# Kernel tuning notes

Measured on AMD Instinct MI355X. Metric: run time of the kernel, lower is better.

## Reference

```python
import jax, jax.numpy as jnp
import numpy as np
import math

B, I, H, NH, HD, OUT = 65536, 256, 64, 8, 8, 64


def _lin(z, W, b):
    # torch nn.Linear convention: W is [out, in]
    return z @ W.T + b


def setup_inputs() -> dict:
    key = jax.random.key(0)
    ks = jax.random.split(key, 30)
    n = lambda i, shape, s=1.0: (jax.random.normal(ks[i], shape, dtype=jnp.float32) * s)
    inp = {
        "x": n(0, (B, I)),
        # _compute_persistence returns random diagrams independent of x; materialized as input
        "persistence": n(1, (I, B, 3, 2)),
        "topo_kernel": n(2, (H, I, 3), 0.05),
        "q_w": n(3, (H, H), 0.05), "q_b": n(4, (H,), 0.05),
        "k_w": n(5, (H, H), 0.05), "k_b": n(6, (H,), 0.05),
        "v_w": n(7, (H, H), 0.05), "v_b": n(8, (H,), 0.05),
        "o_w": n(9, (H, H), 0.05), "o_b": n(10, (H,), 0.05),
        "phase": n(11, (NH,)),
        "update_w": n(12, (H, 2 * H), 0.05), "update_b": n(13, (H,), 0.05),
        "reset_w": n(14, (H, 2 * H), 0.05), "reset_b": n(15, (H,), 0.05),
        "state_w": n(16, (H, 2 * H), 0.05), "state_b": n(17, (H,), 0.05),
        "fisher_m": n(18, (H, H)),
        "metric_m": n(19, (H, H), 0.1),
        "connection": n(20, (H, H, H), 0.01),
        "proj_w": n(21, (H, H), 0.05), "proj_b": n(22, (H,), 0.05),
        "obj_emb": n(23, (H, 64), 0.05),
        "morphisms": n(24, (H, 64, 64), 0.05),
        "functor_w": n(25, (H,)),
        "out_w": n(26, (OUT, 64), 0.05), "out_b": n(27, (OUT,), 0.05),
    }
    return inp


def reference(x, persistence, topo_kernel, q_w, q_b, k_w, k_b, v_w, v_b, o_w, o_b,
              phase, update_w, update_b, reset_w, reset_b, state_w, state_b,
              fisher_m, metric_m, connection, proj_w, proj_b,
              obj_emb, morphisms, functor_w, out_w, out_b):
    # ---- TopologicalConv: out[b,o] = sum_j sum_{d,t} pers[j][b,d,t] * kernel[o,j,d]
    topo = jnp.einsum('jbdt,ojd->bo', persistence, topo_kernel)  # [B, H]

    # ---- QuantumAttentionLayer (seq_len = 1, heads act as the attended axis)
    q = _lin(topo, q_w, q_b).reshape(-1, NH, HD)
    k = _lin(topo, k_w, k_b).reshape(-1, NH, HD)
    v = _lin(topo, v_w, v_b).reshape(-1, NH, HD)
    ph = jnp.exp(1j * phase)[None, :, None]            # per-head phase rotation
    qc = q * ph
    kc = k * jnp.conj(ph)
    scores = jnp.einsum('bhd,bgd->bhg', qc, kc) / math.sqrt(HD)  # [B, NH, NH] complex
    attn = jax.nn.softmax(scores.real, axis=-1) + 1j * jax.nn.softmax(scores.imag, axis=-1)
    av = jnp.einsum('bhg,bgd->bhd', attn, v.astype(attn.dtype))
    quantum = _lin(av.real.reshape(-1, H), o_w, o_b)   # [B, H]

    # ---- InformationRNN single step with h0 = 0
    h0 = jnp.zeros_like(quantum)
    combined = jnp.concatenate([quantum, h0], axis=1)
    update = jax.nn.sigmoid(_lin(combined, update_w, update_b))
    reset = jax.nn.sigmoid(_lin(combined, reset_w, reset_b))
    state_in = jnp.concatenate([quantum, reset * h0], axis=1)
    cand = jnp.tanh(_lin(state_in, state_w, state_b))
    fisher = fisher_m @ fisher_m.T
    nat_grad = jnp.linalg.solve(fisher, (cand - h0).T).T  # fisher @ g = (cand - h)
    new_h = (1.0 - update) * h0 + update * (h0 + nat_grad)

    # ---- ManifoldLayer (geodesic distances are computed-then-discarded in source; skipped)
    metric = metric_m @ metric_m.T
    xm = new_h @ metric
    transported = xm + jnp.einsum('bi,bj,ijk->bk', xm, xm, connection)
    manifold = _lin(transported, proj_w, proj_b)

    # ---- CategoryTheoryNetwork: sum_m softmax(w)_m * (obj @ M_m) == obj @ (sum_m w_m M_m)
    obj = manifold @ obj_emb                     # [B, 64]
    fw = jax.nn.softmax(functor_w)
    m_eff = jnp.einsum('m,mij->ij', fw, morphisms)
    cat = obj @ m_eff                            # [B, 64]

    return _lin(cat, out_w, out_b)               # [B, OUT]
```

## Files before the change

### kernel.cpp

```cpp
#include <hip/hip_runtime.h>
#include <math.h>

typedef float f32x4 __attribute__((ext_vector_type(4)));
typedef __bf16 bf16x8 __attribute__((ext_vector_type(8)));
typedef unsigned short u16x8 __attribute__((ext_vector_type(8)));

__device__ __forceinline__ unsigned short f2bf(float f) {
  unsigned u = __float_as_uint(f);
  return (unsigned short)((u + 0x7fffu + ((u >> 16) & 1u)) >> 16);
}
__device__ __forceinline__ float bf2f(unsigned short s) {
  return __uint_as_float(((unsigned)s) << 16);
}
__device__ __forceinline__ void unpk(unsigned v, float& a, float& b) {
  a = __uint_as_float(v << 16);
  b = __uint_as_float(v & 0xffff0000u);
}
__device__ __forceinline__ bf16x8 ld8bf(const unsigned short* p) {
  uint4 u = *(const uint4*)p;
  return __builtin_bit_cast(bf16x8, u);
}
__device__ __forceinline__ bf16x8 pack8(const float* f) {
  u16x8 t;
#pragma unroll
  for (int i = 0; i < 8; ++i) t[i] = f2bf(f[i]);
  return __builtin_bit_cast(bf16x8, t);
}
__device__ __forceinline__ bf16x8 ld8f32(const float* p) {
  float4 a = *(const float4*)p;
  float4 b = *(const float4*)(p + 4);
  float f[8] = {a.x, a.y, a.z, a.w, b.x, b.y, b.z, b.w};
  return pack8(f);
}
__device__ __forceinline__ f32x4 mfma16(bf16x8 a, bf16x8 b, f32x4 c) {
  return __builtin_amdgcn_mfma_f32_16x16x32_bf16(a, b, c, 0, 0, 0);
}

#define TOPO_OFF   0u
#define CENDT_OFF  8388608u
#define FINV_OFF   8921088u
#define MET_OFF    8929280u
#define WU_OFF     8937472u
#define WC_OFF     8945664u
#define WENDF_OFF  8953856u
#define BU_OFF     8970240u
#define BC_OFF     8970496u
#define BEND_OFF   8970752u
#define COSD_OFF   8971008u

__global__ __launch_bounds__(256, 4) void k_setup_topo(
    const float* __restrict__ pers, const float* __restrict__ tk,
    const float* __restrict__ fisher_m, const float* __restrict__ morphisms,
    const float* __restrict__ functor_w, const float* __restrict__ obj_emb,
    const float* __restrict__ out_w, const float* __restrict__ proj_w,
    const float* __restrict__ proj_b, const float* __restrict__ out_b,
    const float* __restrict__ update_w, const float* __restrict__ update_b,
    const float* __restrict__ state_w, const float* __restrict__ state_b,
    const float* __restrict__ o_w, const float* __restrict__ o_b,
    const float* __restrict__ metric_m, const float* __restrict__ phase,
    char* __restrict__ ws)
{
  __shared__ char smem[33280];
  const int bid = blockIdx.x, tid = threadIdx.x;

  if (bid < 1024) {
    unsigned short* p2 = (unsigned short*)smem;
    const int w = tid >> 6, lane = tid & 63;
    const int m = lane & 15, quad = lane >> 4;
    const size_t b0 = (size_t)bid * 64;
    f32x4 acc[4] = {};
    for (int chunk = 0; chunk < 8; ++chunk) {
      __syncthreads();
#pragma unroll
      for (int rr = 0; rr < 4; ++rr) {
        const int jl = rr * 8 + (tid >> 5);
        const int j = chunk * 32 + jl;
        const int b = (tid & 31) * 2;
        const float4* src = (const float4*)(pers + ((size_t)j * 65536 + b0 + b) * 6);
        float4 f0 = src[0], f1 = src[1], f2c = src[2];
        const int k0 = jl * 3;
        unsigned short* r0p = p2 + b * 104 + k0;
        unsigned short* r1p = p2 + (b + 1) * 104 + k0;
        r0p[0] = f2bf(f0.x + f0.y);
        r0p[1] = f2bf(f0.z + f0.w);
        r0p[2] = f2bf(f1.x + f1.y);
        r1p[0] = f2bf(f1.z + f1.w);
        r1p[1] = f2bf(f2c.x + f2c.y);
        r1p[2] = f2bf(f2c.z + f2c.w);
      }
      __syncthreads();
#pragma unroll
      for (int ks = 0; ks < 3; ++ks) {
        bf16x8 a = ld8bf(p2 + (w * 16 + m) * 104 + ks * 32 + quad * 8);
        const int kg = chunk * 96 + ks * 32 + quad * 8;
#pragma unroll
        for (int nt = 0; nt < 4; ++nt) {
          bf16x8 bb = ld8f32(tk + (nt * 16 + m) * 768 + kg);
          acc[nt] = mfma16(a, bb, acc[nt]);
        }
      }
    }
    unsigned short* topo_bf = (unsigned short*)(ws + TOPO_OFF);
#pragma unroll
    for (int nt = 0; nt < 4; ++nt)
#pragma unroll
      for (int r = 0; r < 4; ++r)
        topo_bf[(b0 + w * 16 + quad * 4 + r) * 64 + nt * 16 + m] = f2bf(acc[nt][r]);

  } else if (bid == 1024) {
    float* aug = (float*)smem;
    for (int e = tid; e < 4096; e += 256) {
      const int r = e >> 6, c = e & 63;
      float s = 0.f;
      for (int l = 0; l < 64; ++l) s += fisher_m[r * 64 + l] * fisher_m[c * 64 + l];
      aug[r * 130 + c] = s;
      aug[r * 130 + 64 + c] = (r == c) ? 1.f : 0.f;
    }
    __syncthreads();
    const int rr = tid >> 2, cs = tid & 3;
    for (int p = 0; p < 64; ++p) {
      const float piv = 1.f / aug[p * 130 + p];
      const float f = (rr != p) ? aug[rr * 130 + p] : 0.f;
      __syncthreads();
      if (tid < 130) aug[p * 130 + tid] *= piv;
      __syncthreads();
      if (rr != p)
        for (int c = cs; c < 130; c += 4)
          aug[rr * 130 + c] -= f * aug[p * 130 + c];
      __syncthreads();
    }
    unsigned short* finv = (unsigned short*)(ws + FINV_OFF);
    for (int e = tid; e < 4096; e += 256)
      finv[e] = f2bf(aug[(e >> 6) * 130 + 64 + (e & 63)]);

  } else if (bid == 1025) {
    float* L0 = (float*)smem;
    float* L1s = (float*)(smem + 16384);
    float* fw = (float*)(smem + 32768);
    if (tid < 64) {
      float mx = functor_w[0];
      for (int i2 = 1; i2 < 64; ++i2) mx = fmaxf(mx, functor_w[i2]);
      float se = 0.f;
      for (int i2 = 0; i2 < 64; ++i2) se += expf(functor_w[i2] - mx);
      fw[tid] = expf(functor_w[tid] - mx) / se;
    }
    __syncthreads();
    for (int e = tid; e < 4096; e += 256) {
      const int p = e >> 6, q = e & 63;
      float s = 0.f;
      for (int m2 = 0; m2 < 64; ++m2) s += fw[m2] * morphisms[m2 * 4096 + p * 64 + q];
      L0[e] = s;
    }
    __syncthreads();
    for (int e = tid; e < 4096; e += 256) {
      const int mm2 = e >> 6, q = e & 63;
      float s = 0.f;
      for (int p = 0; p < 64; ++p) s += obj_emb[mm2 * 64 + p] * L0[p * 64 + q];
      L1s[e] = s;
    }
    __syncthreads();
    for (int e = tid; e < 4096; e += 256) {
      const int mm2 = e >> 6, n = e & 63;
      float s = 0.f;
      for (int q = 0; q < 64; ++q) s += L1s[mm2 * 64 + q] * out_w[n * 64 + q];
      L0[e] = s;
    }
    __syncthreads();
    float* wendf = (float*)(ws + WENDF_OFF);
    for (int e = tid; e < 4096; e += 256) {
      const int kp = e >> 6, n = e & 63;
      float s = 0.f;
      for (int m2 = 0; m2 < 64; ++m2) s += proj_w[m2 * 64 + kp] * L0[m2 * 64 + n];
      wendf[e] = s;
    }
    if (tid < 64) {
      float s = out_b[tid];
      for (int m2 = 0; m2 < 64; ++m2) s += proj_b[m2] * L0[m2 * 64 + tid];
      ((float*)(ws + BEND_OFF))[tid] = s;
    }

  } else {
    unsigned short* wu = (unsigned short*)(ws + WU_OFF);
    unsigned short* wc = (unsigned short*)(ws + WC_OFF);
    unsigned short* met = (unsigned short*)(ws + MET_OFF);
    for (int e = tid; e < 4096; e += 256) {
      const int n = e >> 6, k2 = e & 63;
      float su = 0.f, sc = 0.f, sm = 0.f;
      for (int m2 = 0; m2 < 64; ++m2) {
        const float ow = o_w[m2 * 64 + k2];
        su += update_w[n * 128 + m2] * ow;
        sc += state_w[n * 128 + m2] * ow;
        sm += metric_m[n * 64 + m2] * metric_m[k2 * 64 + m2];
      }
      wu[e] = f2bf(su); wc[e] = f2bf(sc); met[e] = f2bf(sm);
    }
    if (tid < 64) {
      float s1 = update_b[tid], s2 = state_b[tid];
      for (int m2 = 0; m2 < 64; ++m2) {
        const float ob = o_b[m2];
        s1 += update_w[tid * 128 + m2] * ob;
        s2 += state_w[tid * 128 + m2] * ob;
      }
      ((float*)(ws + BU_OFF))[tid] = s1;
      ((float*)(ws + BC_OFF))[tid] = s2;
    } else if (tid < 128) {
      const int e = tid - 64;
      ((float*)(ws + COSD_OFF))[e] =
          cosf(phase[e >> 3] - phase[e & 7]) * 0.35355339059327376f;
    }
  }
}

__global__ __launch_bounds__(256) void k_cend(const float* __restrict__ conn,
                                              char* __restrict__ ws)
{
  __shared__ float wl[4096];
  const int bid = blockIdx.x, tid = threadIdx.x;
  unsigned short* cendt = (unsigned short*)(ws + CENDT_OFF);
  const float* wendf = (const float*)(ws + WENDF_OFF);
  if (bid < 64) {
    for (int e = tid; e < 4096; e += 256) wl[e] = wendf[e];
    __syncthreads();
    const int i = bid;
    const int j = tid >> 2, nb = tid & 3;
    float cr[64];
    const float* cp = conn + ((size_t)i * 64 + j) * 64;
#pragma unroll
    for (int kp = 0; kp < 64; ++kp) cr[kp] = cp[kp];
    for (int n = nb * 16; n < nb * 16 + 16; ++n) {
      float s = 0.f;
#pragma unroll
      for (int kp = 0; kp < 64; ++kp) s += cr[kp] * wl[kp * 64 + n];
      cendt[(size_t)n * 4160 + i * 64 + j] = f2bf(s);
    }
  } else {
    for (int e = tid; e < 4096; e += 256) {
      const int i2 = e >> 6, n = e & 63;
      cendt[(size_t)n * 4160 + 4096 + i2] = f2bf(wendf[i2 * 64 + n]);
    }
  }
}

__global__ __launch_bounds__(256, 2) void k_main(
    const float* __restrict__ q_w, const float* __restrict__ q_b,
    const float* __restrict__ k_w, const float* __restrict__ k_b,
    const float* __restrict__ v_w, const float* __restrict__ v_b,
    const char* __restrict__ ws, float* __restrict__ out)
{
  __shared__ char smem[73728];
  unsigned short* S0 = (unsigned short*)smem;
  unsigned short* S1 = (unsigned short*)(smem + 18432);
  unsigned short* S2 = (unsigned short*)(smem + 36864);
  unsigned short* S3 = (unsigned short*)(smem + 55296);
  const int tid = threadIdx.x;
  const int w = tid >> 6, lane = tid & 63;
  const int m = lane & 15, quad = lane >> 4;
  const size_t r0 = (size_t)blockIdx.x * 128;
  const unsigned short* topo_bf = (const unsigned short*)(ws + TOPO_OFF);
  const unsigned short* CENDT = (const unsigned short*)(ws + CENDT_OFF);
  const unsigned short* FINV = (const unsigned short*)(ws + FINV_OFF);
  const unsigned short* MET = (const unsigned short*)(ws + MET_OFF);
  const unsigned short* WU = (const unsigned short*)(ws + WU_OFF);
  const unsigned short* WC = (const unsigned short*)(ws + WC_OFF);
  const float* BU = (const float*)(ws + BU_OFF);
  const float* BC = (const float*)(ws + BC_OFF);
  const float* BEND = (const float*)(ws + BEND_OFF);
  const float* COSD = (const float*)(ws + COSD_OFF);

  {
    const float* Wp[3] = {q_w, k_w, v_w};
    const float* Bp[3] = {q_b, k_b, v_b};
    unsigned short* Dp[3] = {S0, S1, S2};
#pragma unroll
    for (int g3 = 0; g3 < 3; ++g3) {
      bf16x8 bfr[2][4];
#pragma unroll
      for (int ks = 0; ks < 2; ++ks)
#pragma unroll
        for (int nt = 0; nt < 4; ++nt)
          bfr[ks][nt] = ld8f32(Wp[g3] + (nt * 16 + m) * 64 + ks * 32 + quad * 8);
      float bias[4];
#pragma unroll
      for (int nt = 0; nt < 4; ++nt) bias[nt] = Bp[g3][nt * 16 + m];
#pragma unroll
      for (int mi = 0; mi < 2; ++mi) {
        const int mt = w * 2 + mi;
        f32x4 acc[4] = {};
#pragma unroll
        for (int ks = 0; ks < 2; ++ks) {
          bf16x8 a = ld8bf(topo_bf + (r0 + mt * 16 + m) * 64 + ks * 32 + quad * 8);
#pragma unroll
          for (int nt = 0; nt < 4; ++nt) acc[nt] = mfma16(a, bfr[ks][nt], acc[nt]);
        }
#pragma unroll
        for (int nt = 0; nt < 4; ++nt)
#pragma unroll
          for (int r = 0; r < 4; ++r)
            Dp[g3][(mt * 16 + quad * 4 + r) * 72 + nt * 16 + m] =
                f2bf(acc[nt][r] + bias[nt]);
      }
    }
  }
  __syncthreads();

  {
    const int bl = tid >> 1, hh = (tid & 1) * 4;
    float kvv[64];
    const uint4* krow = (const uint4*)(S1 + bl * 72);
#pragma unroll
    for (int x = 0; x < 8; ++x) {
      uint4 u = krow[x];
      unpk(u.x, kvv[x * 8 + 0], kvv[x * 8 + 1]);
      unpk(u.y, kvv[x * 8 + 2], kvv[x * 8 + 3]);
      unpk(u.z, kvv[x * 8 + 4], kvv[x * 8 + 5]);
      unpk(u.w, kvv[x * 8 + 6], kvv[x * 8 + 7]);
    }
    const uint4* qrow = (const uint4*)(S0 + bl * 72);
    const uint4* vrow = (const uint4*)(S2 + bl * 72);
#pragma unroll
    for (int hi = 0; hi < 4; ++hi) {
      const int h = hh + hi;
      float qv[8];
      {
        uint4 u = qrow[h];
        unpk(u.x, qv[0], qv[1]); unpk(u.y, qv[2], qv[3]);
        unpk(u.z, qv[4], qv[5]); unpk(u.w, qv[6], qv[7]);
      }
      float s[8];
#pragma unroll
      for (int g = 0; g < 8; ++g) {
        float a = 0.f;
#pragma unroll
        for (int d = 0; d < 8; ++d) a += qv[d] * kvv[g * 8 + d];
        s[g] = a * COSD[h * 8 + g];
      }
      float mx = s[0];
#pragma unroll
      for (int g = 1; g < 8; ++g) mx = fmaxf(mx, s[g]);
      float se = 0.f;
#pragma unroll
      for (int g = 0; g < 8; ++g) { s[g] = expf(s[g] - mx); se += s[g]; }
      const float inv = 1.f / se;
      float av[8] = {};
#pragma unroll
      for (int g = 0; g < 8; ++g) {
        const float ag = s[g] * inv;
        float vg[8];
        uint4 u = vrow[g];
        unpk(u.x, vg[0], vg[1]); unpk(u.y, vg[2], vg[3]);
        unpk(u.z, vg[4], vg[5]); unpk(u.w, vg[6], vg[7]);
#pragma unroll
        for (int d = 0; d < 8; ++d) av[d] += ag * vg[d];
      }
      unsigned int* dstp = (unsigned int*)(S3 + bl * 72 + h * 8);
#pragma unroll
      for (int d2 = 0; d2 < 4; ++d2)
        dstp[d2] = (unsigned)f2bf(av[2 * d2]) | ((unsigned)f2bf(av[2 * d2 + 1]) << 16);
    }
  }
  __syncthreads();

  {
#pragma unroll
    for (int g2 = 0; g2 < 2; ++g2) {
      const unsigned short* wp = g2 ? WC : WU;
      const float* bp = g2 ? BC : BU;
      unsigned short* dst = g2 ? S1 : S0;
      bf16x8 bfr[2][4];
#pragma unroll
      for (int ks = 0; ks < 2; ++ks)
#pragma unroll
        for (int nt = 0; nt < 4; ++nt)
          bfr[ks][nt] = ld8bf(wp + (nt * 16 + m) * 64 + ks * 32 + quad * 8);
      float bias[4];
#pragma unroll
      for (int nt = 0; nt < 4; ++nt) bias[nt] = bp[nt * 16 + m];
#pragma unroll
      for (int mi = 0; mi < 2; ++mi) {
        const int mt = w * 2 + mi;
        f32x4 acc[4] = {};
#pragma unroll
        for (int ks = 0; ks < 2; ++ks) {
          bf16x8 a = ld8bf(S3 + (mt * 16 + m) * 72 + ks * 32 + quad * 8);
#pragma unroll
          for (int nt = 0; nt < 4; ++nt) acc[nt] = mfma16(a, bfr[ks][nt], acc[nt]);
        }
#pragma unroll
        for (int nt = 0; nt < 4; ++nt)
#pragma unroll
          for (int r = 0; r < 4; ++r) {
            const float x = acc[nt][r] + bias[nt];
            const float y = g2 ? tanhf(x) : 1.f / (1.f + expf(-x));
            dst[(mt * 16 + quad * 4 + r) * 72 + nt * 16 + m] = f2bf(y);
          }
      }
    }
  }
  __syncthreads();

  {
    bf16x8 bfr[2][4];
#pragma unroll
    for (int ks = 0; ks < 2; ++ks)
#pragma unroll
      for (int nt = 0; nt < 4; ++nt)
        bfr[ks][nt] = ld8bf(FINV + (nt * 16 + m) * 64 + ks * 32 + quad * 8);
#pragma unroll
    for (int mi = 0; mi < 2; ++mi) {
      const int mt = w * 2 + mi;
      f32x4 acc[4] = {};
#pragma unroll
      for (int ks = 0; ks < 2; ++ks) {
        bf16x8 a = ld8bf(S1 + (mt * 16 + m) * 72 + ks * 32 + quad * 8);
#pragma unroll
        for (int nt = 0; nt < 4; ++nt) acc[nt] = mfma16(a, bfr[ks][nt], acc[nt]);
      }
#pragma unroll
      for (int nt = 0; nt < 4; ++nt)
#pragma unroll
        for (int r = 0; r < 4; ++r) {
          const int row = mt * 16 + quad * 4 + r, col = nt * 16 + m;
          const float u = bf2f(S0[row * 72 + col]);
          S2[row * 72 + col] = f2bf(u * acc[nt][r]);
        }
    }
  }
  __syncthreads();

  {
    float* XM = (float*)smem;
    bf16x8 bfr[2][4];
#pragma unroll
    for (int ks = 0; ks < 2; ++ks)
#pragma unroll
      for (int nt = 0; nt < 4; ++nt)
        bfr[ks][nt] = ld8bf(MET + (nt * 16 + m) * 64 + ks * 32 + quad * 8);
#pragma unroll
    for (int mi = 0; mi < 2; ++mi) {
      const int mt = w * 2 + mi;
      f32x4 acc[4] = {};
#pragma unroll
      for (int ks = 0; ks < 2; ++ks) {
        bf16x8 a = ld8bf(S2 + (mt * 16 + m) * 72 + ks * 32 + quad * 8);
#pragma unroll
        for (int nt = 0; nt < 4; ++nt) acc[nt] = mfma16(a, bfr[ks][nt], acc[nt]);
      }
#pragma unroll
      for (int nt = 0; nt < 4; ++nt)
#pragma unroll
        for (int r = 0; r < 4; ++r)
          XM[(mt * 16 + quad * 4 + r) * 68 + nt * 16 + m] = acc[nt][r];
    }
  }
  __syncthreads();

  {
    float* XM = (float*)smem;
    unsigned short* stg = (unsigned short*)(smem + 36864);
    float seg[2][2][8];
#pragma unroll
    for (int mi = 0; mi < 2; ++mi) {
      const int brow = w * 32 + mi * 16 + m;
#pragma unroll
      for (int s = 0; s < 2; ++s)
#pragma unroll
        for (int jj = 0; jj < 8; ++jj)
          seg[mi][s][jj] = XM[brow * 68 + s * 32 + quad * 8 + jj];
    }
    f32x4 acc2[2][4] = {};

    auto stage = [&](int cc, int half) {
#pragma unroll
      for (int ks = 0; ks < 4; ++ks) {
        const unsigned short* gp =
            CENDT + (size_t)(w * 16 + m) * 4160 + cc * 128 + ks * 32 + quad * 8;
        const char* lp = smem + 36864 + half * 16384 + (ks * 4 + w) * 1024;
        __builtin_amdgcn_global_load_lds(
            (const __attribute__((address_space(1))) unsigned int*)gp,
            (__attribute__((address_space(3))) unsigned int*)lp, 16, 0, 0);
      }
    };

    stage(0, 0);
    for (int cc = 0; cc < 32; ++cc) {
      __syncthreads();
      if (cc + 1 < 32) stage(cc + 1, (cc + 1) & 1);
      const unsigned short* buf = stg + (cc & 1) * 8192;
#pragma unroll
      for (int ks = 0; ks < 4; ++ks) {
        const int i = cc * 2 + (ks >> 1);
        const int s = ks & 1;
        bf16x8 afr[2];
#pragma unroll
        for (int mi = 0; mi < 2; ++mi) {
          const float xi = XM[(w * 32 + mi * 16 + m) * 68 + i];
          float pr[8];
#pragma unroll
          for (int jj = 0; jj < 8; ++jj) pr[jj] = xi * seg[mi][s][jj];
          afr[mi] = pack8(pr);
        }
#pragma unroll
        for (int nt = 0; nt < 4; ++nt) {
          bf16x8 bfr = ld8bf(buf + (ks * 4 + nt) * 512 + lane * 8);
          acc2[0][nt] = mfma16(afr[0], bfr, acc2[0][nt]);
          acc2[1][nt] = mfma16(afr[1], bfr, acc2[1][nt]);
        }
      }
    }
#pragma unroll
    for (int ks = 0; ks < 2; ++ks) {
      bf16x8 afr[2];
#pragma unroll
      for (int mi = 0; mi < 2; ++mi) afr[mi] = pack8(seg[mi][ks]);
#pragma unroll
      for (int nt = 0; nt < 4; ++nt) {
        bf16x8 bfr =
            ld8bf(CENDT + (size_t)(nt * 16 + m) * 4160 + 4096 + ks * 32 + quad * 8);
        acc2[0][nt] = mfma16(afr[0], bfr, acc2[0][nt]);
        acc2[1][nt] = mfma16(afr[1], bfr, acc2[1][nt]);
      }
    }
    float bendv[4];
#pragma unroll
    for (int nt = 0; nt < 4; ++nt) bendv[nt] = BEND[nt * 16 + m];
#pragma unroll
    for (int mi = 0; mi < 2; ++mi)
#pragma unroll
      for (int nt = 0; nt < 4; ++nt)
#pragma unroll
        for (int r = 0; r < 4; ++r)
          out[(r0 + (w * 2 + mi) * 16 + quad * 4 + r) * 64 + nt * 16 + m] =
              acc2[mi][nt][r] + bendv[nt];
  }
}

extern "C" void kernel_launch(void* const* d_in, const int* in_sizes, int n_in,
                              void* d_out, int out_size, void* d_ws, size_t ws_size,
                              hipStream_t stream) {
  (void)in_sizes; (void)n_in; (void)out_size; (void)ws_size;
  const float* pers     = (const float*)d_in[1];
  const float* tk       = (const float*)d_in[2];
  const float* q_w      = (const float*)d_in[3];
  const float* q_b      = (const float*)d_in[4];
  const float* k_w      = (const float*)d_in[5];
  const float* k_b      = (const float*)d_in[6];
  const float* v_w      = (const float*)d_in[7];
  const float* v_b      = (const float*)d_in[8];
  const float* o_w      = (const float*)d_in[9];
  const float* o_b      = (const float*)d_in[10];
  const float* phase    = (const float*)d_in[11];
  const float* update_w = (const float*)d_in[12];
  const float* update_b = (const float*)d_in[13];
  const float* state_w  = (const float*)d_in[16];
  const float* state_b  = (const float*)d_in[17];
  const float* fisher_m = (const float*)d_in[18];
  const float* metric_m = (const float*)d_in[19];
  const float* conn     = (const float*)d_in[20];
  const float* proj_w   = (const float*)d_in[21];
  const float* proj_b   = (const float*)d_in[22];
  const float* obj_emb  = (const float*)d_in[23];
  const float* morph    = (const float*)d_in[24];
  const float* funct_w  = (const float*)d_in[25];
  const float* out_w    = (const float*)d_in[26];
  const float* out_b    = (const float*)d_in[27];
  char* ws = (char*)d_ws;

  hipLaunchKernelGGL(k_setup_topo, dim3(1027), dim3(256), 0, stream,
                     pers, tk, fisher_m, morph, funct_w, obj_emb, out_w, proj_w,
                     proj_b, out_b, update_w, update_b, state_w, state_b, o_w,
                     o_b, metric_m, phase, ws);
  hipLaunchKernelGGL(k_cend, dim3(65), dim3(256), 0, stream, conn, ws);
  hipLaunchKernelGGL(k_main, dim3(512), dim3(256), 0, stream,
                     q_w, q_b, k_w, k_b, v_w, v_b, (const char*)ws,
                     (float*)d_out);
}
```

Baseline: 922.8 us.

## Load persistence directly into MFMA registers and prepack topo kernel to bf16

The topological conv stage no longer stages persistence through shared memory with block barriers. Each lane loads its own row's persistence values straight into registers, prefetching the next k-step while the current MFMA runs, and pads each group of 3 to 4 so a K-slice of 8 covers two j indices. A new small kernel pre-converts topo_kernel into a padded bf16 layout in workspace, replacing per-iteration fp32 loads and conversions. In exchange the global reads are small float2 loads per lane (64 rows times stride 24 bytes) instead of wide float4 loads, there is an extra kernel launch, and the MFMA work grows by a third because of the zero padding.

```diff
diff --git a/kernel.cpp b/kernel.cpp
--- a/kernel.cpp
+++ b/kernel.cpp
@@ -47,6 +47,15 @@
 #define BC_OFF     8970496u
 #define BEND_OFF   8970752u
 #define COSD_OFF   8971008u
+#define TKP_OFF    8971264u
+
+__global__ __launch_bounds__(256) void k_pretk(const float* __restrict__ tk,
+                                               char* __restrict__ ws) {
+  const int e = blockIdx.x * 256 + threadIdx.x;
+  const int o = e >> 10, kk = e & 1023, j = kk >> 2, d = kk & 3;
+  const float v = (d < 3) ? tk[((size_t)o * 256 + j) * 3 + d] : 0.f;
+  ((unsigned short*)(ws + TKP_OFF))[e] = f2bf(v);
+}
 
 __global__ __launch_bounds__(256, 4) void k_setup_topo(
     const float* __restrict__ pers, const float* __restrict__ tk,
@@ -64,40 +73,45 @@
   const int bid = blockIdx.x, tid = threadIdx.x;
 
   if (bid < 1024) {
-    unsigned short* p2 = (unsigned short*)smem;
     const int w = tid >> 6, lane = tid & 63;
     const int m = lane & 15, quad = lane >> 4;
-    const size_t b0 = (size_t)bid * 64;
+    const size_t rowbase = (size_t)bid * 64 + w * 16;
+    const size_t b = rowbase + m;
+    const unsigned short* tkp = (const unsigned short*)(ws + TKP_OFF);
+    const float* pbase = pers + b * 6;
+
     f32x4 acc[4] = {};
-    for (int chunk = 0; chunk < 8; ++chunk) {
-      __syncthreads();
-#pragma unroll
-      for (int rr = 0; rr < 4; ++rr) {
-        const int jl = rr * 8 + (tid >> 5);
-        const int j = chunk * 32 + jl;
-        const int b = (tid & 31) * 2;
-        const float4* src = (const float4*)(pers + ((size_t)j * 65536 + b0 + b) * 6);
-        float4 f0 = src[0], f1 = src[1], f2c = src[2];
-        const int k0 = jl * 3;
-        unsigned short* r0p = p2 + b * 104 + k0;
-        unsigned short* r1p = p2 + (b + 1) * 104 + k0;
-        r0p[0] = f2bf(f0.x + f0.y);
-        r0p[1] = f2bf(f0.z + f0.w);
-        r0p[2] = f2bf(f1.x + f1.y);
-        r1p[0] = f2bf(f1.z + f1.w);
-        r1p[1] = f2bf(f2c.x + f2c.y);
-        r1p[2] = f2bf(f2c.z + f2c.w);
-      }
-      __syncthreads();
-#pragma unroll
-      for (int ks = 0; ks < 3; ++ks) {
-        bf16x8 a = ld8bf(p2 + (w * 16 + m) * 104 + ks * 32 + quad * 8);
-        const int kg = chunk * 96 + ks * 32 + quad * 8;
-#pragma unroll
-        for (int nt = 0; nt < 4; ++nt) {
-          bf16x8 bb = ld8f32(tk + (nt * 16 + m) * 768 + kg);
-          acc[nt] = mfma16(a, bb, acc[nt]);
-        }
+    float2 c0, c1, c2, c3, c4, c5;
+    {
+      const float* p0 = pbase + (size_t)(quad * 2) * 393216;
+      c0 = *(const float2*)(p0);
+      c1 = *(const float2*)(p0 + 2);
+      c2 = *(const float2*)(p0 + 4);
+      const float* p1 = p0 + 393216;
+      c3 = *(const float2*)(p1);
+      c4 = *(const float2*)(p1 + 2);
+      c5 = *(const float2*)(p1 + 4);
+    }
+    for (int ks = 0; ks < 32; ++ks) {
+      float f[8] = {c0.x + c0.y, c1.x + c1.y, c2.x + c2.y, 0.f,
+                    c3.x + c3.y, c4.x + c4.y, c5.x + c5.y, 0.f};
+      bf16x8 a = pack8(f);
+      if (ks + 1 < 32) {
+        const int jn = (ks + 1) * 8 + quad * 2;
+        const float* p0 = pbase + (size_t)jn * 393216;
+        c0 = *(const float2*)(p0);
+        c1 = *(const float2*)(p0 + 2);
+        c2 = *(const float2*)(p0 + 4);
+        const float* p1 = p0 + 393216;
+        c3 = *(const float2*)(p1);
+        c4 = *(const float2*)(p1 + 2);
+        c5 = *(const float2*)(p1 + 4);
+      }
+      const unsigned short* bk = tkp + ks * 32 + quad * 8;
+#pragma unroll
+      for (int nt = 0; nt < 4; ++nt) {
+        bf16x8 bb = ld8bf(bk + (size_t)(nt * 16 + m) * 1024);
+        acc[nt] = mfma16(a, bb, acc[nt]);
       }
     }
     unsigned short* topo_bf = (unsigned short*)(ws + TOPO_OFF);
@@ -105,7 +119,7 @@
     for (int nt = 0; nt < 4; ++nt)
 #pragma unroll
       for (int r = 0; r < 4; ++r)
-        topo_bf[(b0 + w * 16 + quad * 4 + r) * 64 + nt * 16 + m] = f2bf(acc[nt][r]);
+        topo_bf[(rowbase + quad * 4 + r) * 64 + nt * 16 + m] = f2bf(acc[nt][r]);
 
   } else if (bid == 1024) {
     float* aug = (float*)smem;
@@ -565,6 +579,7 @@
   const float* out_b    = (const float*)d_in[27];
   char* ws = (char*)d_ws;
 
+  hipLaunchKernelGGL(k_pretk, dim3(256), dim3(256), 0, stream, tk, ws);
   hipLaunchKernelGGL(k_setup_topo, dim3(1027), dim3(256), 0, stream,
                      pers, tk, fisher_m, morph, funct_w, obj_emb, out_w, proj_w,
                      proj_b, out_b, update_w, update_b, state_w, state_b, o_w,
```

New measurement: 871.4 us. 1.06x faster.

## Split topo conv into register-pipelined kernel with pre-packed bf16 weight fragments

Applied to the files above, without the earlier changes.

Moves the topological convolution out of the setup kernel into its own kernel. That kernel loads persistence pairs straight into MFMA A-fragments in registers, without an LDS staging pass or block barriers, and software-pipelines the global loads several k-steps ahead. A new pre-pass packs topo_kernel into bf16 B-fragment layout (K padded from 3 to 4) so the main loop reads ready-made fragments instead of converting fp32 weights each step. This adds one kernel launch and spends some MFMA work on zero padding, in return for removing the barriers and LDS traffic on a read of about 400 MB of persistence data.

```diff
diff --git a/kernel.cpp b/kernel.cpp
--- a/kernel.cpp
+++ b/kernel.cpp
@@ -25,6 +25,12 @@
 #pragma unroll
   for (int i = 0; i < 8; ++i) t[i] = f2bf(f[i]);
   return __builtin_bit_cast(bf16x8, t);
+}
+__device__ __forceinline__ bf16x8 pack8c(const float* f) {
+  bf16x8 r;
+#pragma unroll
+  for (int i = 0; i < 8; ++i) r[i] = (__bf16)f[i];
+  return r;
 }
 __device__ __forceinline__ bf16x8 ld8f32(const float* p) {
   float4 a = *(const float4*)p;
@@ -47,9 +53,10 @@
 #define BC_OFF     8970496u
 #define BEND_OFF   8970752u
 #define COSD_OFF   8971008u
-
-__global__ __launch_bounds__(256, 4) void k_setup_topo(
-    const float* __restrict__ pers, const float* __restrict__ tk,
+#define TKB_OFF    8971264u
+
+__global__ __launch_bounds__(256) void k_pre(
+    const float* __restrict__ tk,
     const float* __restrict__ fisher_m, const float* __restrict__ morphisms,
     const float* __restrict__ functor_w, const float* __restrict__ obj_emb,
     const float* __restrict__ out_w, const float* __restrict__ proj_w,
@@ -63,51 +70,17 @@
   __shared__ char smem[33280];
   const int bid = blockIdx.x, tid = threadIdx.x;
 
-  if (bid < 1024) {
-    unsigned short* p2 = (unsigned short*)smem;
-    const int w = tid >> 6, lane = tid & 63;
-    const int m = lane & 15, quad = lane >> 4;
-    const size_t b0 = (size_t)bid * 64;
-    f32x4 acc[4] = {};
-    for (int chunk = 0; chunk < 8; ++chunk) {
-      __syncthreads();
-#pragma unroll
-      for (int rr = 0; rr < 4; ++rr) {
-        const int jl = rr * 8 + (tid >> 5);
-        const int j = chunk * 32 + jl;
-        const int b = (tid & 31) * 2;
-        const float4* src = (const float4*)(pers + ((size_t)j * 65536 + b0 + b) * 6);
-        float4 f0 = src[0], f1 = src[1], f2c = src[2];
-        const int k0 = jl * 3;
-        unsigned short* r0p = p2 + b * 104 + k0;
-        unsigned short* r1p = p2 + (b + 1) * 104 + k0;
-        r0p[0] = f2bf(f0.x + f0.y);
-        r0p[1] = f2bf(f0.z + f0.w);
-        r0p[2] = f2bf(f1.x + f1.y);
-        r1p[0] = f2bf(f1.z + f1.w);
-        r1p[1] = f2bf(f2c.x + f2c.y);
-        r1p[2] = f2bf(f2c.z + f2c.w);
-      }
-      __syncthreads();
-#pragma unroll
-      for (int ks = 0; ks < 3; ++ks) {
-        bf16x8 a = ld8bf(p2 + (w * 16 + m) * 104 + ks * 32 + quad * 8);
-        const int kg = chunk * 96 + ks * 32 + quad * 8;
-#pragma unroll
-        for (int nt = 0; nt < 4; ++nt) {
-          bf16x8 bb = ld8f32(tk + (nt * 16 + m) * 768 + kg);
-          acc[nt] = mfma16(a, bb, acc[nt]);
-        }
-      }
-    }
-    unsigned short* topo_bf = (unsigned short*)(ws + TOPO_OFF);
-#pragma unroll
-    for (int nt = 0; nt < 4; ++nt)
-#pragma unroll
-      for (int r = 0; r < 4; ++r)
-        topo_bf[(b0 + w * 16 + quad * 4 + r) * 64 + nt * 16 + m] = f2bf(acc[nt][r]);
-
-  } else if (bid == 1024) {
+  if (bid < 256) {
+    const int E = bid * 256 + tid;
+    const int i = E & 7, nt = (E >> 3) & 3, m = (E >> 5) & 15;
+    const int quad = (E >> 9) & 3, ks = E >> 11;
+    const int o = nt * 16 + m;
+    const int k = ks * 32 + quad * 8 + i;
+    const int j = k >> 2, d = k & 3;
+    const float v = (d < 3) ? tk[((size_t)o * 256 + j) * 3 + d] : 0.f;
+    ((unsigned short*)(ws + TKB_OFF))[E] = f2bf(v);
+
+  } else if (bid == 256) {
     float* aug = (float*)smem;
     for (int e = tid; e < 4096; e += 256) {
       const int r = e >> 6, c = e & 63;
@@ -133,7 +106,7 @@
     for (int e = tid; e < 4096; e += 256)
       finv[e] = f2bf(aug[(e >> 6) * 130 + 64 + (e & 63)]);
 
-  } else if (bid == 1025) {
+  } else if (bid == 257) {
     float* L0 = (float*)smem;
     float* L1s = (float*)(smem + 16384);
     float* fw = (float*)(smem + 32768);
@@ -209,6 +182,107 @@
           cosf(phase[e >> 3] - phase[e & 7]) * 0.35355339059327376f;
     }
   }
+}
+
+__global__ __launch_bounds__(256, 4) void k_topo(const float* __restrict__ pers,
+                                                 char* __restrict__ ws)
+{
+  const int tid = threadIdx.x;
+  const int w = tid >> 6, lane = tid & 63;
+  const int m = lane & 15, quad = lane >> 4;
+  const size_t rowbase = (size_t)blockIdx.x * 64 + w * 16;
+  const int b = (int)rowbase + m;
+  const unsigned short* tkB = (const unsigned short*)(ws + TKB_OFF);
+  const float* pers_l = pers + (size_t)(quad * 2) * 393216 + (size_t)b * 6;
+  const size_t tkb_l = (size_t)(quad * 16 + m) * 32;
+
+  f32x4 acc[4] = {};
+  float2 c[4][6];
+  bf16x8 Bf[2][4];
+
+#define LOADP(KI, KS)                                                    \
+  {                                                                      \
+    const float* p0 = pers_l + (size_t)(KS) * 3145728;                   \
+    c[KI][0] = *(const float2*)(p0);                                     \
+    c[KI][1] = *(const float2*)(p0 + 2);                                 \
+    c[KI][2] = *(const float2*)(p0 + 4);                                 \
+    const float* p1 = p0 + 393216;                                       \
+    c[KI][3] = *(const float2*)(p1);                                     \
+    c[KI][4] = *(const float2*)(p1 + 2);                                 \
+    c[KI][5] = *(const float2*)(p1 + 4);                                 \
+  }
+#define LOADB(SL, KS)                                                    \
+  {                                                                      \
+    const unsigned short* bp = tkB + tkb_l + (size_t)(KS) * 2048;        \
+    Bf[SL][0] = ld8bf(bp);                                               \
+    Bf[SL][1] = ld8bf(bp + 8);                                           \
+    Bf[SL][2] = ld8bf(bp + 16);                                          \
+    Bf[SL][3] = ld8bf(bp + 24);                                          \
+  }
+
+  LOADB(0, 0)
+  LOADB(1, 1)
+  LOADP(0, 0)
+  LOADP(1, 1)
+  LOADP(2, 2)
+  LOADP(3, 3)
+
+  for (int kb = 0; kb < 7; ++kb) {
+#pragma unroll
+    for (int ki = 0; ki < 4; ++ki) {
+      const int ks = kb * 4 + ki;
+      float f[8];
+      f[0] = c[ki][0].x + c[ki][0].y;
+      f[1] = c[ki][1].x + c[ki][1].y;
+      f[2] = c[ki][2].x + c[ki][2].y;
+      f[3] = 0.f;
+      f[4] = c[ki][3].x + c[ki][3].y;
+      f[5] = c[ki][4].x + c[ki][4].y;
+      f[6] = c[ki][5].x + c[ki][5].y;
+      f[7] = 0.f;
+      bf16x8 a = pack8c(f);
+      const int slot = ki & 1;
+      bf16x8 B0 = Bf[slot][0], B1 = Bf[slot][1];
+      bf16x8 B2 = Bf[slot][2], B3 = Bf[slot][3];
+      LOADB(slot, ks + 2)
+      LOADP(ki, ks + 4)
+      acc[0] = mfma16(a, B0, acc[0]);
+      acc[1] = mfma16(a, B1, acc[1]);
+      acc[2] = mfma16(a, B2, acc[2]);
+      acc[3] = mfma16(a, B3, acc[3]);
+    }
+  }
+#pragma unroll
+  for (int ki = 0; ki < 4; ++ki) {
+    const int ks = 28 + ki;
+    float f[8];
+    f[0] = c[ki][0].x + c[ki][0].y;
+    f[1] = c[ki][1].x + c[ki][1].y;
+    f[2] = c[ki][2].x + c[ki][2].y;
+    f[3] = 0.f;
+    f[4] = c[ki][3].x + c[ki][3].y;
+    f[5] = c[ki][4].x + c[ki][4].y;
+    f[6] = c[ki][5].x + c[ki][5].y;
+    f[7] = 0.f;
+    bf16x8 a = pack8c(f);
+    const int slot = ki & 1;
+    bf16x8 B0 = Bf[slot][0], B1 = Bf[slot][1];
+    bf16x8 B2 = Bf[slot][2], B3 = Bf[slot][3];
+    if (ks + 2 < 32) LOADB(slot, ks + 2)
+    acc[0] = mfma16(a, B0, acc[0]);
+    acc[1] = mfma16(a, B1, acc[1]);
+    acc[2] = mfma16(a, B2, acc[2]);
+    acc[3] = mfma16(a, B3, acc[3]);
+  }
+#undef LOADP
+#undef LOADB
+
+  unsigned short* topo_bf = (unsigned short*)(ws + TOPO_OFF);
+#pragma unroll
+  for (int nt = 0; nt < 4; ++nt)
+#pragma unroll
+    for (int r = 0; r < 4; ++r)
+      topo_bf[(rowbase + quad * 4 + r) * 64 + nt * 16 + m] = f2bf(acc[nt][r]);
 }
 
 __global__ __launch_bounds__(256) void k_cend(const float* __restrict__ conn,
@@ -565,10 +639,11 @@
   const float* out_b    = (const float*)d_in[27];
   char* ws = (char*)d_ws;
 
-  hipLaunchKernelGGL(k_setup_topo, dim3(1027), dim3(256), 0, stream,
-                     pers, tk, fisher_m, morph, funct_w, obj_emb, out_w, proj_w,
+  hipLaunchKernelGGL(k_pre, dim3(259), dim3(256), 0, stream,
+                     tk, fisher_m, morph, funct_w, obj_emb, out_w, proj_w,
                      proj_b, out_b, update_w, update_b, state_w, state_b, o_w,
                      o_b, metric_m, phase, ws);
+  hipLaunchKernelGGL(k_topo, dim3(1024), dim3(256), 0, stream, pers, ws);
   hipLaunchKernelGGL(k_cend, dim3(65), dim3(256), 0, stream, conn, ws);
   hipLaunchKernelGGL(k_main, dim3(512), dim3(256), 0, stream,
                      q_w, q_b, k_w, k_b, v_w, v_b, (const char*)ws,
```

New measurement: 875.2 us. 1.05x faster.
